# Performance work log

Measured on AMD Instinct MI355X. Metric: run time of the kernel, lower is better.

## Reference

```python
import jax, jax.numpy as jnp
import numpy as np

D_MODEL = 1024
NUM_HEADS = 16
HEAD_DIM = D_MODEL // NUM_HEADS


def setup_inputs() -> dict:
    key = jax.random.key(0)
    ks = jax.random.split(key, 5)
    scale = 1.0 / np.sqrt(D_MODEL)
    x = jax.random.normal(ks[0], (2, 2048, D_MODEL), dtype=jnp.float32)
    W_qkv = jax.random.normal(ks[1], (D_MODEL, 3 * D_MODEL), dtype=jnp.float32) * scale
    b_qkv = jnp.zeros((3 * D_MODEL,), dtype=jnp.float32)
    W_proj = jax.random.normal(ks[2], (D_MODEL, D_MODEL), dtype=jnp.float32) * scale
    b_proj = jnp.zeros((D_MODEL,), dtype=jnp.float32)
    return {"x": x, "W_qkv": W_qkv, "b_qkv": b_qkv, "W_proj": W_proj, "b_proj": b_proj}


def reference(x, W_qkv, b_qkv, W_proj, b_proj):
    B, S, D = x.shape
    qkv = x @ W_qkv + b_qkv                      # [B,S,3D]
    qkv = qkv.reshape(B, S, 3, NUM_HEADS, HEAD_DIM)
    qkv = jnp.transpose(qkv, (2, 0, 3, 1, 4))    # [3,B,H,S,hd]
    q, k, v = qkv[0], qkv[1], qkv[2]
    scores = jnp.einsum('bhqd,bhkd->bhqk', q, k) / jnp.sqrt(jnp.asarray(HEAD_DIM, x.dtype))
    probs = jax.nn.softmax(scores, axis=-1)
    out = jnp.einsum('bhqk,bhkd->bhqd', probs, v)  # [B,H,S,hd]
    out = jnp.transpose(out, (0, 2, 1, 3)).reshape(B, S, D)
    return out @ W_proj + b_proj
```

## Files before the change

kernel.cpp:

```cpp
#include <hip/hip_runtime.h>
#include <math.h>

#define B_ 2
#define S_ 2048
#define D_ 1024
#define H_ 16
#define HD_ 64

typedef __bf16 bf16x8 __attribute__((ext_vector_type(8)));
typedef __bf16 bf16x4 __attribute__((ext_vector_type(4)));
typedef __bf16 bf16x2 __attribute__((ext_vector_type(2)));
typedef float f32x4 __attribute__((ext_vector_type(4)));
typedef float f32x16 __attribute__((ext_vector_type(16)));
typedef unsigned u32x2 __attribute__((ext_vector_type(2)));

#define GLOAD16(gsrc, ldst) \
  __builtin_amdgcn_global_load_lds((const __attribute__((address_space(1))) void*)(gsrc), \
                                   (__attribute__((address_space(3))) void*)(ldst), 16, 0, 0)

#define QSCALE 0.18033688f

static __device__ __forceinline__ unsigned pack2(float a, float b) {
    bf16x2 v; v[0] = (__bf16)a; v[1] = (__bf16)b;
    return __builtin_bit_cast(unsigned, v);
}

__global__ __launch_bounds__(256) void conv_k(
    const float* __restrict__ in, __bf16* __restrict__ out)
{
    int i = (blockIdx.x * 256 + threadIdx.x) * 8;
    float4 a = *(const float4*)(in + i);
    float4 b = *(const float4*)(in + i + 4);
    bf16x8 v;
    v[0] = (__bf16)a.x; v[1] = (__bf16)a.y; v[2] = (__bf16)a.z; v[3] = (__bf16)a.w;
    v[4] = (__bf16)b.x; v[5] = (__bf16)b.y; v[6] = (__bf16)b.z; v[7] = (__bf16)b.w;
    *(bf16x8*)(out + i) = v;
}

__global__ __launch_bounds__(256) void transpose_bf16_k(
    const float* __restrict__ in, __bf16* __restrict__ t_out, int K, int N,
    int qcols, float qs)
{
    __shared__ float t[64][65];
    const int tid = threadIdx.x;
    const int bj = blockIdx.x * 64;
    const int bi = blockIdx.y * 64;
    #pragma unroll
    for (int it = 0; it < 4; ++it) {
        int idx = (tid + it * 256) * 4;
        int r = idx >> 6, c = idx & 63;
        float4 v = *(const float4*)(in + (size_t)(bi + r) * N + bj + c);
        t[r][c] = v.x; t[r][c+1] = v.y; t[r][c+2] = v.z; t[r][c+3] = v.w;
    }
    __syncthreads();
    int j = tid & 63;
    int i0 = (tid >> 6) * 16;
    float s = (bj + j) < qcols ? qs : 1.0f;
    bf16x8 h0, h1;
    #pragma unroll
    for (int ii = 0; ii < 8; ++ii) h0[ii] = (__bf16)(t[i0 + ii][j] * s);
    #pragma unroll
    for (int ii = 0; ii < 8; ++ii) h1[ii] = (__bf16)(t[i0 + 8 + ii][j] * s);
    size_t o = (size_t)(bj + j) * K + bi + i0;
    *(bf16x8*)(t_out + o) = h0; *(bf16x8*)(t_out + o + 8) = h1;
}

template<typename OutT>
__global__ __launch_bounds__(256) void gemm_nt_k(
    const __bf16* __restrict__ A, const __bf16* __restrict__ Bt,
    const float* __restrict__ bias, OutT* __restrict__ C,
    int M, int N, int K, int qcols, float qs)
{
    constexpr int TSZ = 128 * 64;
    __shared__ __bf16 sA[TSZ];
    __shared__ __bf16 sB[TSZ];

    const int tid = threadIdx.x, w = tid >> 6, l = tid & 63;
    const int lr = l & 15, lg = l >> 4;
    const int bm = blockIdx.y * 128, bn = blockIdx.x * 128;
    const int wm = w >> 1, wn = w & 1;

    f32x4 acc[4][4] = {};

    for (int k0 = 0; k0 < K; k0 += 64) {
        __syncthreads();
        #pragma unroll
        for (int c = 0; c < 4; ++c) {
            int q = w * 4 + c;
            int r = q * 8 + (l >> 3);
            int sl = ((l & 7) ^ (r & 7)) * 8;
            GLOAD16(A + (size_t)(bm + r) * K + k0 + sl, sA + q * 512);
            GLOAD16(Bt + (size_t)(bn + r) * K + k0 + sl, sB + q * 512);
        }
        __syncthreads();
        #pragma unroll
        for (int kk = 0; kk < 2; ++kk) {
            bf16x8 ah[4], bh[4];
            #pragma unroll
            for (int i = 0; i < 4; ++i) {
                int ra = wm * 64 + i * 16 + lr;
                int sa = ((kk * 4 + lg) ^ (ra & 7)) * 8;
                ah[i] = *(const bf16x8*)(sA + ra * 64 + sa);
                int rb = wn * 64 + i * 16 + lr;
                int sb = ((kk * 4 + lg) ^ (rb & 7)) * 8;
                bh[i] = *(const bf16x8*)(sB + rb * 64 + sb);
            }
            #pragma unroll
            for (int mi = 0; mi < 4; ++mi)
                #pragma unroll
                for (int ni = 0; ni < 4; ++ni)
                    acc[mi][ni] = __builtin_amdgcn_mfma_f32_16x16x32_bf16(ah[mi], bh[ni], acc[mi][ni], 0, 0, 0);
        }
    }

    #pragma unroll
    for (int ni = 0; ni < 4; ++ni) {
        int col = bn + wn * 64 + ni * 16 + lr;
        float bv = bias[col];
        if (col < qcols) bv *= qs;
        #pragma unroll
        for (int mi = 0; mi < 4; ++mi) {
            #pragma unroll
            for (int r = 0; r < 4; ++r) {
                int row = bm + wm * 64 + mi * 16 + lg * 4 + r;
                float v = acc[mi][ni][r] + bv;
                C[(size_t)row * N + col] = (OutT)v;
            }
        }
    }
}

__global__ __launch_bounds__(512) void attn32_k(
    const __bf16* __restrict__ qkv, __bf16* __restrict__ attn)
{
    __shared__ __bf16 Ks[2][2][64 * 64];
    __shared__ __bf16 Vt[2][2][64 * 64];

    const int tid = threadIdx.x, w = tid >> 6, l = tid & 63;
    const int q32 = l & 31, hi = l >> 5;
    const int bid = blockIdx.x;
    const int qt = bid >> 5, hb = bid & 31;
    const int h = hb >> 1, b = hb & 1;
    const int q0 = qt * 256;
    const size_t ldq = 3 * D_;
    const __bf16* Qg = qkv + (size_t)b * S_ * ldq + h * HD_;
    const __bf16* Kg = Qg + D_;
    const __bf16* Vg = Qg + 2 * D_;
    const int qg = q0 + w * 32 + q32;

    bf16x8 qf[4];
    #pragma unroll
    for (int ds = 0; ds < 4; ++ds)
        qf[ds] = *(const bf16x8*)(Qg + (size_t)qg * ldq + ds * 16 + hi * 8);

    const int krow = tid >> 3;
    const int ksl  = (tid & 7) ^ (krow & 7);
    const int vk   = tid & 63;
    const int vd0  = (tid >> 6) * 8;
    int voff[8];
    #pragma unroll
    for (int j = 0; j < 8; ++j)
        voff[j] = (vd0 + j) * 128 + (((vk >> 3) ^ j) * 16) + (vk & 7) * 2;

    f32x16 o[2] = {};
    float lsum = 0.f;
    bf16x8 vrA, vrB;

    auto stageK = [&](int kt, int set, int t) {
        GLOAD16(Kg + (size_t)(kt * 64 + krow) * ldq + ksl * 8, &Ks[set][t][w * 512]);
    };
    auto loadV = [&](int kt) {
        return *(const bf16x8*)(Vg + (size_t)(kt * 64 + vk) * ldq + vd0);
    };
    auto writeV = [&](int set, int t, const bf16x8& vr) {
        #pragma unroll
        for (int j = 0; j < 8; ++j)
            *(__bf16*)((char*)&Vt[set][t][0] + voff[j]) = vr[j];
    };

    auto computeTile = [&](int set, int t) {
        f32x16 sc[2] = {};
        __builtin_amdgcn_s_setprio(1);
        #pragma unroll
        for (int kb = 0; kb < 2; ++kb) {
            int r = kb * 32 + q32;
            #pragma unroll
            for (int ds = 0; ds < 4; ++ds) {
                int slot = (ds * 2 + hi) ^ (r & 7);
                bf16x8 kf = *(const bf16x8*)((const char*)&Ks[set][t][0] + r * 128 + slot * 16);
                sc[kb] = __builtin_amdgcn_mfma_f32_32x32x16_bf16(kf, qf[ds], sc[kb], 0, 0, 0);
            }
        }
        __builtin_amdgcn_s_setprio(0);

        float sum = 0.f;
        #pragma unroll
        for (int kb = 0; kb < 2; ++kb)
            #pragma unroll
            for (int i = 0; i < 16; ++i) {
                float pv = exp2f(sc[kb][i]);
                sc[kb][i] = pv;
                sum += pv;
            }
        lsum += sum;

        bf16x8 pa[2][2];
        #pragma unroll
        for (int kb = 0; kb < 2; ++kb) {
            #pragma unroll
            for (int tl = 0; tl < 2; ++tl) {
                int base = tl * 8;
                unsigned A0 = pack2(sc[kb][base + 0], sc[kb][base + 1]);
                unsigned A1 = pack2(sc[kb][base + 2], sc[kb][base + 3]);
                unsigned B0 = pack2(sc[kb][base + 4], sc[kb][base + 5]);
                unsigned B1 = pack2(sc[kb][base + 6], sc[kb][base + 7]);
                u32x2 s0 = __builtin_amdgcn_permlane32_swap(A0, B0, false, false);
                u32x2 s1 = __builtin_amdgcn_permlane32_swap(A1, B1, false, false);
                union { unsigned u[4]; bf16x8 v; } pu;
                pu.u[0] = s0[0]; pu.u[1] = s1[0]; pu.u[2] = s0[1]; pu.u[3] = s1[1];
                pa[kb][tl] = pu.v;
            }
        }

        __builtin_amdgcn_s_setprio(1);
        #pragma unroll
        for (int db = 0; db < 2; ++db) {
            int dr = db * 32 + q32;
            #pragma unroll
            for (int tt = 0; tt < 4; ++tt) {
                int slot = (tt * 2 + hi) ^ (dr & 7);
                bf16x8 vf = *(const bf16x8*)((const char*)&Vt[set][t][0] + dr * 128 + slot * 16);
                o[db] = __builtin_amdgcn_mfma_f32_32x32x16_bf16(vf, pa[tt >> 1][tt & 1], o[db], 0, 0, 0);
            }
        }
        __builtin_amdgcn_s_setprio(0);
    };

    stageK(0, 0, 0); stageK(1, 0, 1);
    vrA = loadV(0);  vrB = loadV(1);
    writeV(0, 0, vrA); writeV(0, 1, vrB);
    __syncthreads();

    constexpr int NP = S_ / 128;
    for (int pr = 0; pr < NP; ++pr) {
        const int set = pr & 1, nset = set ^ 1;
        if (pr < NP - 1) {
            stageK(2 * pr + 2, nset, 0);
            stageK(2 * pr + 3, nset, 1);
            vrA = loadV(2 * pr + 2);
            vrB = loadV(2 * pr + 3);
        }
        computeTile(set, 0);
        computeTile(set, 1);
        if (pr < NP - 1) {
            writeV(nset, 0, vrA);
            writeV(nset, 1, vrB);
        }
        __syncthreads();
    }

    lsum += __shfl_xor(lsum, 32);
    float inv = 1.0f / lsum;
    #pragma unroll
    for (int db = 0; db < 2; ++db)
        #pragma unroll
        for (int rg = 0; rg < 4; ++rg) {
            int d = db * 32 + 8 * rg + 4 * hi;
            bf16x4 ov;
            #pragma unroll
            for (int i = 0; i < 4; ++i) ov[i] = (__bf16)(o[db][rg * 4 + i] * inv);
            *(bf16x4*)(attn + ((size_t)b * S_ + qg) * D_ + h * HD_ + d) = ov;
        }
}

extern "C" void kernel_launch(void* const* d_in, const int* in_sizes, int n_in,
                              void* d_out, int out_size, void* d_ws, size_t ws_size,
                              hipStream_t stream) {
    const float* x     = (const float*)d_in[0];
    const float* Wqkv  = (const float*)d_in[1];
    const float* bqkv  = (const float*)d_in[2];
    const float* Wproj = (const float*)d_in[3];
    const float* bproj = (const float*)d_in[4];

    __bf16* ws = (__bf16*)d_ws;
    const size_t MB = 1024 * 1024 / 2;
    __bf16* x_bf  = ws;
    __bf16* wq_t  = x_bf + 8 * MB;
    __bf16* wp_t  = wq_t + 6 * MB;
    __bf16* qkv   = wp_t + 2 * MB;
    __bf16* attn  = qkv + 24 * MB;

    const int M = B_ * S_;

    conv_k<<<2048, 256, 0, stream>>>(x, x_bf);
    transpose_bf16_k<<<dim3(48, 16), 256, 0, stream>>>(Wqkv, wq_t, D_, 3 * D_, D_, QSCALE);
    transpose_bf16_k<<<dim3(16, 16), 256, 0, stream>>>(Wproj, wp_t, D_, D_, 0, 1.0f);

    gemm_nt_k<__bf16><<<dim3(24, 32), 256, 0, stream>>>(
        x_bf, wq_t, bqkv, qkv, M, 3 * D_, D_, D_, QSCALE);

    attn32_k<<<256, 512, 0, stream>>>(qkv, attn);

    gemm_nt_k<float><<<dim3(8, 32), 256, 0, stream>>>(
        attn, wp_t, bproj, (float*)d_out, M, D_, D_, 0, 1.0f);
}
```

Before: 147.7 us.

## Split attention KV range across two blocks and combine partial outputs

The attention grid doubles from 256 to 512 blocks, and each block processes half of the key/value sequence. Each block writes unnormalized bf16 partial outputs and row sums to workspace. A new combine kernel adds the two halves and normalizes. This raises parallelism on a GPU with many compute units, at the cost of an extra launch, extra global traffic and one more bf16 rounding of the partials. The exp2f call is also swapped for the hardware exp2 builtin. Workspace buffers are reordered so the partials reuse the x_bf/wq_t region.

Measured after the change: 140.9 us. 4.6% less time.

```diff
diff --git a/kernel.cpp b/kernel.cpp
--- a/kernel.cpp
+++ b/kernel.cpp
@@ -131,7 +131,8 @@
 }
 
 __global__ __launch_bounds__(512) void attn32_k(
-    const __bf16* __restrict__ qkv, __bf16* __restrict__ attn)
+    const __bf16* __restrict__ qkv, __bf16* __restrict__ Pout,
+    float* __restrict__ Lout)
 {
     __shared__ __bf16 Ks[2][2][64 * 64];
     __shared__ __bf16 Vt[2][2][64 * 64];
@@ -139,9 +140,11 @@
     const int tid = threadIdx.x, w = tid >> 6, l = tid & 63;
     const int q32 = l & 31, hi = l >> 5;
     const int bid = blockIdx.x;
-    const int qt = bid >> 5, hb = bid & 31;
+    const int X = bid >> 5, hb = bid & 31;
+    const int qt = X >> 1, kvh = X & 1;
     const int h = hb >> 1, b = hb & 1;
     const int q0 = qt * 256;
+    const int kvbase = kvh * 1024;
     const size_t ldq = 3 * D_;
     const __bf16* Qg = qkv + (size_t)b * S_ * ldq + h * HD_;
     const __bf16* Kg = Qg + D_;
@@ -166,11 +169,12 @@
     float lsum = 0.f;
     bf16x8 vrA, vrB;
 
-    auto stageK = [&](int kt, int set, int t) {
-        GLOAD16(Kg + (size_t)(kt * 64 + krow) * ldq + ksl * 8, &Ks[set][t][w * 512]);
+    auto stageK = [&](int lt, int set, int t) {
+        GLOAD16(Kg + (size_t)(kvbase + lt * 64 + krow) * ldq + ksl * 8,
+                &Ks[set][t][w * 512]);
     };
-    auto loadV = [&](int kt) {
-        return *(const bf16x8*)(Vg + (size_t)(kt * 64 + vk) * ldq + vd0);
+    auto loadV = [&](int lt) {
+        return *(const bf16x8*)(Vg + (size_t)(kvbase + lt * 64 + vk) * ldq + vd0);
     };
     auto writeV = [&](int set, int t, const bf16x8& vr) {
         #pragma unroll
@@ -198,7 +202,7 @@
         for (int kb = 0; kb < 2; ++kb)
             #pragma unroll
             for (int i = 0; i < 16; ++i) {
-                float pv = exp2f(sc[kb][i]);
+                float pv = __builtin_amdgcn_exp2f(sc[kb][i]);
                 sc[kb][i] = pv;
                 sum += pv;
             }
@@ -241,7 +245,7 @@
     writeV(0, 0, vrA); writeV(0, 1, vrB);
     __syncthreads();
 
-    constexpr int NP = S_ / 128;
+    constexpr int NP = 8;
     for (int pr = 0; pr < NP; ++pr) {
         const int set = pr & 1, nset = set ^ 1;
         if (pr < NP - 1) {
@@ -260,7 +264,8 @@
     }
 
     lsum += __shfl_xor(lsum, 32);
-    float inv = 1.0f / lsum;
+    const size_t orow = (size_t)b * S_ + qg;
+    __bf16* Pb = Pout + (size_t)kvh * (4096 * 1024) + orow * D_ + h * HD_;
     #pragma unroll
     for (int db = 0; db < 2; ++db)
         #pragma unroll
@@ -268,9 +273,30 @@
             int d = db * 32 + 8 * rg + 4 * hi;
             bf16x4 ov;
             #pragma unroll
-            for (int i = 0; i < 4; ++i) ov[i] = (__bf16)(o[db][rg * 4 + i] * inv);
-            *(bf16x4*)(attn + ((size_t)b * S_ + qg) * D_ + h * HD_ + d) = ov;
-        }
+            for (int i = 0; i < 4; ++i) ov[i] = (__bf16)o[db][rg * 4 + i];
+            *(bf16x4*)(Pb + d) = ov;
+        }
+    if (hi == 0)
+        Lout[(size_t)kvh * (4096 * 16) + orow * 16 + h] = lsum;
+}
+
+__global__ __launch_bounds__(256) void combine_k(
+    const __bf16* __restrict__ P, const float* __restrict__ L,
+    __bf16* __restrict__ attnb)
+{
+    int i = (blockIdx.x * 256 + threadIdx.x) * 8;
+    int row = i >> 10;
+    int h = (i & 1023) >> 6;
+    float l0 = L[row * 16 + h];
+    float l1 = L[4096 * 16 + row * 16 + h];
+    float inv = 1.0f / (l0 + l1);
+    bf16x8 p0 = *(const bf16x8*)(P + i);
+    bf16x8 p1 = *(const bf16x8*)(P + 4096 * 1024 + i);
+    bf16x8 r;
+    #pragma unroll
+    for (int j = 0; j < 8; ++j)
+        r[j] = (__bf16)(((float)p0[j] + (float)p1[j]) * inv);
+    *(bf16x8*)(attnb + i) = r;
 }
 
 extern "C" void kernel_launch(void* const* d_in, const int* in_sizes, int n_in,
@@ -283,12 +309,14 @@
     const float* bproj = (const float*)d_in[4];
 
     __bf16* ws = (__bf16*)d_ws;
-    const size_t MB = 1024 * 1024 / 2;
-    __bf16* x_bf  = ws;
-    __bf16* wq_t  = x_bf + 8 * MB;
-    __bf16* wp_t  = wq_t + 6 * MB;
-    __bf16* qkv   = wp_t + 2 * MB;
-    __bf16* attn  = qkv + 24 * MB;
+    const size_t MB = 524288;
+    __bf16* wp_t  = ws;
+    __bf16* qkv   = ws + 2 * MB;
+    __bf16* attnb = ws + 26 * MB;
+    __bf16* x_bf  = ws + 34 * MB;
+    __bf16* wq_t  = ws + 42 * MB;
+    __bf16* Pp    = ws + 34 * MB;
+    float*  Lp    = (float*)(ws + 50 * MB);
 
     const int M = B_ * S_;
 
@@ -299,8 +327,10 @@
     gemm_nt_k<__bf16><<<dim3(24, 32), 256, 0, stream>>>(
         x_bf, wq_t, bqkv, qkv, M, 3 * D_, D_, D_, QSCALE);
 
-    attn32_k<<<256, 512, 0, stream>>>(qkv, attn);
+    attn32_k<<<512, 512, 0, stream>>>(qkv, Pp, Lp);
+
+    combine_k<<<2048, 256, 0, stream>>>(Pp, Lp, attnb);
 
     gemm_nt_k<float><<<dim3(8, 32), 256, 0, stream>>>(
-        attn, wp_t, bproj, (float*)d_out, M, D_, D_, 0, 1.0f);
-}
+        attnb, wp_t, bproj, (float*)d_out, M, D_, D_, 0, 1.0f);
+}
```
